# Kernel optimization log

Hardware: AMD Instinct MI355X
Metric: run time of the kernel (lower is better)

Reference implementation:

```python
import jax, jax.numpy as jnp
import numpy as np

B=4; TEXT_LEN=64; IMG=256; P=16; DIM=1024; HEADS=16; LAYERS=2; MLP=4; VOCAB=50000; TDIM=256; MAXTXT=2048
HP=IMG//P; NPATCH=HP*HP; HD=DIM//HEADS; EPS=1e-5

def _ln(x, g, b):
    m = jnp.mean(x, -1, keepdims=True)
    v = jnp.mean((x - m) ** 2, -1, keepdims=True)
    return (x - m) / jnp.sqrt(v + EPS) * g + b

def _rope_cos_sin(n, d):
    inv = 1.0 / (10000.0 ** (jnp.arange(0, d, 2, dtype=jnp.float32) / d))
    f = jnp.outer(jnp.arange(n, dtype=jnp.float32), inv)
    e = jnp.concatenate([f, f], -1)  # [n, d]
    return jnp.cos(e), jnp.sin(e)

def _rot_half(x):
    # matches torch: cat((-x[...,1::2], x[...,::2]), -1)
    return jnp.concatenate([-x[..., 1::2], x[..., ::2]], -1)

def _forward(noisy_images, text_tokens, timesteps, W_tok, pos_text, W_patch, pos_img, cls_tok,
             W_t1, b_t1, W_t2, b_t2, ln1_g, ln1_b, Wq, Wk, Wv, Wo, ln2_g, ln2_b,
             Wm1, Wm2, Wada, b_ada, fn_g, fn_b, W_final, b_final):
    Bn = noisy_images.shape[0]
    # text embed: one_hot @ W_tok.T == gather of columns of W_tok [DIM, VOCAB]
    text_emb = jnp.transpose(jnp.take(W_tok, text_tokens, axis=1), (1, 2, 0)) + pos_text[:, :TEXT_LEN]
    # image patches: [B,3,HP,P,HP,P] -> [B,HP,WP,C,P,P] -> [B,NPATCH, 3*P*P]
    patches = noisy_images.reshape(Bn, 3, HP, P, HP, P).transpose(0, 2, 4, 1, 3, 5).reshape(Bn, NPATCH, 3 * P * P)
    img_emb = patches @ W_patch.T + pos_img
    img_emb = jnp.concatenate([jnp.broadcast_to(cls_tok, (Bn, 1, DIM)), img_emb], 1)
    x = jnp.concatenate([text_emb, img_emb], 1)  # [B, N, DIM]
    N = x.shape[1]
    # sinusoidal timestep embedding (dim=256)
    half = TDIM // 2
    freqs = jnp.exp(-jnp.log(10000.0) * jnp.arange(half, dtype=jnp.float32) / half)
    args = timesteps.astype(jnp.float32)[:, None] * freqs[None]
    temb_raw = jnp.concatenate([jnp.cos(args), jnp.sin(args)], -1)
    t_emb = jax.nn.silu(temb_raw @ W_t1.T + b_t1) @ W_t2.T + b_t2  # [B, DIM]
    cos, sin = _rope_cos_sin(N, HD)
    scale = HD ** -0.5
    for l in range(LAYERS):
        mod = jax.nn.silu(t_emb) @ Wada[l].T + b_ada[l]
        sh_msa, sc_msa, g_msa, sh_mlp, sc_mlp, g_mlp = jnp.split(mod, 6, -1)
        xn = _ln(x, ln1_g[l], ln1_b[l]) * (1 + sc_msa[:, None]) + sh_msa[:, None]
        q = (xn @ Wq[l].T).reshape(Bn, N, HEADS, HD).transpose(0, 2, 1, 3)
        k = (xn @ Wk[l].T).reshape(Bn, N, HEADS, HD).transpose(0, 2, 1, 3)
        v = (xn @ Wv[l].T).reshape(Bn, N, HEADS, HD).transpose(0, 2, 1, 3)
        q = q * cos + _rot_half(q) * sin
        k = k * cos + _rot_half(k) * sin
        att = jax.nn.softmax(jnp.einsum('bhnd,bhmd->bhnm', q, k) * scale, -1)
        o = jnp.einsum('bhnm,bhmd->bhnd', att, v).transpose(0, 2, 1, 3).reshape(Bn, N, DIM)
        x = x + g_msa[:, None] * (o @ Wo[l].T)
        xn2 = _ln(x, ln2_g[l], ln2_b[l]) * (1 + sc_mlp[:, None]) + sh_mlp[:, None]
        mlp = jax.nn.gelu(xn2 @ Wm1[l].T, approximate=False) @ Wm2[l].T
        x = x + g_mlp[:, None] * mlp
    img_tok = x[:, TEXT_LEN + 1:]
    out = _ln(img_tok, fn_g, fn_b) @ W_final.T + b_final  # [B, NPATCH, 3*P*P]
    out = out.reshape(Bn, HP, HP, 3, P, P).transpose(0, 3, 1, 4, 2, 5).reshape(Bn, 3, IMG, IMG)
    return out

def setup_inputs() -> dict:
    key = jax.random.key(0)
    ks = jax.random.split(key, 24)
    def n(k, shape, s=0.02):
        return (jax.random.normal(k, shape, jnp.float32) * s).astype(jnp.float32)
    inp = {}
    inp['noisy_images'] = jax.random.normal(ks[0], (B, 3, IMG, IMG), jnp.float32)
    inp['text_tokens'] = jax.random.randint(ks[1], (B, TEXT_LEN), 0, VOCAB)
    inp['timesteps'] = jax.random.randint(ks[2], (B,), 0, 1000)
    inp['W_tok'] = n(ks[3], (DIM, VOCAB))
    inp['pos_text'] = n(ks[4], (1, MAXTXT, DIM))
    inp['W_patch'] = n(ks[5], (DIM, 3 * P * P))
    inp['pos_img'] = n(ks[6], (1, NPATCH, DIM))
    inp['cls_tok'] = n(ks[7], (1, 1, DIM))
    inp['W_t1'] = n(ks[8], (DIM, TDIM)); inp['b_t1'] = jnp.zeros((DIM,), jnp.float32)
    inp['W_t2'] = n(ks[9], (DIM, DIM)); inp['b_t2'] = jnp.zeros((DIM,), jnp.float32)
    inp['ln1_g'] = jnp.ones((LAYERS, DIM), jnp.float32); inp['ln1_b'] = jnp.zeros((LAYERS, DIM), jnp.float32)
    inp['Wq'] = n(ks[10], (LAYERS, DIM, DIM))
    inp['Wk'] = n(ks[11], (LAYERS, DIM, DIM))
    inp['Wv'] = n(ks[12], (LAYERS, DIM, DIM))
    inp['Wo'] = n(ks[13], (LAYERS, DIM, DIM))
    inp['ln2_g'] = jnp.ones((LAYERS, DIM), jnp.float32); inp['ln2_b'] = jnp.zeros((LAYERS, DIM), jnp.float32)
    inp['Wm1'] = n(ks[14], (LAYERS, MLP * DIM, DIM))
    inp['Wm2'] = n(ks[15], (LAYERS, DIM, MLP * DIM))
    inp['Wada'] = n(ks[16], (LAYERS, 6 * DIM, DIM)); inp['b_ada'] = jnp.zeros((LAYERS, 6 * DIM), jnp.float32)
    inp['fn_g'] = jnp.ones((DIM,), jnp.float32); inp['fn_b'] = jnp.zeros((DIM,), jnp.float32)
    inp['W_final'] = n(ks[17], (3 * P * P, DIM)); inp['b_final'] = jnp.zeros((3 * P * P,), jnp.float32)
    return inp

def reference(noisy_images, text_tokens, timesteps, W_tok, pos_text, W_patch, pos_img, cls_tok,
              W_t1, b_t1, W_t2, b_t2, ln1_g, ln1_b, Wq, Wk, Wv, Wo, ln2_g, ln2_b,
              Wm1, Wm2, Wada, b_ada, fn_g, fn_b, W_final, b_final):
    return _forward(noisy_images, text_tokens, timesteps, W_tok, pos_text, W_patch, pos_img, cls_tok,
                    W_t1, b_t1, W_t2, b_t2, ln1_g, ln1_b, Wq, Wk, Wv, Wo, ln2_g, ln2_b,
                    Wm1, Wm2, Wada, b_ada, fn_g, fn_b, W_final, b_final)
```

## Files before the change

kernel.cpp:

```cpp
#include <hip/hip_runtime.h>
#include <math.h>

constexpr int kBn    = 4;
constexpr int kText  = 64;
constexpr int kImg   = 256;
constexpr int kDim   = 1024;
constexpr int kHeads = 16;
constexpr int kHd    = 64;
constexpr int kNp    = 256;
constexpr int kTok   = 321;
constexpr int kVocab = 50000;
constexpr int kTdim  = 256;
constexpr int kMlp   = 4096;
constexpr int kScLd  = 384;
constexpr int kScRow = 384;
constexpr float kEps = 1e-5f;

typedef __attribute__((ext_vector_type(8))) short short8;
typedef __attribute__((ext_vector_type(4))) float f32x4;

__device__ __forceinline__ short f2bf(float x) {
  unsigned u = __builtin_bit_cast(unsigned, x);
  unsigned r = (u + 0x7FFFu + ((u >> 16) & 1u)) >> 16;
  return (short)r;
}

__device__ __forceinline__ void glds16(const short* g, short* l) {
  __builtin_amdgcn_global_load_lds(
      (const __attribute__((address_space(1))) unsigned int*)g,
      (__attribute__((address_space(3))) unsigned int*)l, 16, 0, 0);
}

struct GemmM {
  const short* A; const short* B; float* C; const float* E;
  int M, N, K, lda, ldb, ldc;
  long sA0, sA1, sB0, sB1, sC0, sC1;
  int innerB, ldE, rowsPB;
  float alpha;
  int nSplit, splitLen;
  long partStride;
};

__device__ __forceinline__ float epi_apply(int EPI, const GemmM& p, const float* E,
                                           long co, int gm, int gn, float v) {
  if (EPI == 1) v += E[gn];
  else if (EPI == 3) v = 0.5f*v*(1.f + erff(v*0.70710678118654752f));
  else if (EPI == 4) v += E[(long)gm*p.ldE + gn];
  else if (EPI == 5) v = p.C[co] + E[(long)(gm / p.rowsPB)*p.ldE + gn] * v;
  return v;
}

template<int EPI, bool PART, bool OUTBF>
__global__ __launch_bounds__(256) void gemm_gl(GemmM p) {
  int bz = blockIdx.z;
  int split = 0;
  if (PART) { split = bz % p.nSplit; bz /= p.nSplit; }
  int b1 = bz % p.innerB, b0 = bz / p.innerB;
  const short* A = p.A + b0*p.sA0 + b1*p.sA1;
  const short* B = p.B + b0*p.sB0 + b1*p.sB1;
  long cbase = b0*p.sC0 + b1*p.sC1 + (PART ? (long)split * p.partStride : 0);
  const float* E = p.E;

  int kBeg = PART ? split * p.splitLen : 0;
  int kEnd = PART ? min(p.K, kBeg + p.splitLen) : p.K;

  __shared__ short As[2][64*64];
  __shared__ short Bs[2][64*64];

  int tid  = threadIdx.x;
  int lane = tid & 63, widx = tid >> 6;
  int quad = lane >> 4, ln = lane & 15;
  int wm = (widx >> 1) * 32, wn = (widx & 1) * 32;
  int n0 = blockIdx.x * 64, m0 = blockIdx.y * 64;

  int l3 = lane >> 3, l7 = lane & 7;
  int kofs = (l7 ^ l3) * 8;
  const short* gA0 = A + (long)(m0 + 16*widx + l3) * p.lda + kofs;
  const short* gA1 = gA0 + (long)8 * p.lda;
  const short* gB0 = B + (long)(n0 + 16*widx + l3) * p.ldb + kofs;
  const short* gB1 = gB0 + (long)8 * p.ldb;
  short* lA0 = &As[0][(2*widx)*512];
  short* lA1 = &As[0][(2*widx+1)*512];
  short* lB0 = &Bs[0][(2*widx)*512];
  short* lB1 = &Bs[0][(2*widx+1)*512];

  auto stage = [&](int buf, int k0) {
    int bo = buf * 4096;
    glds16(gA0 + k0, lA0 + bo);
    glds16(gA1 + k0, lA1 + bo);
    glds16(gB0 + k0, lB0 + bo);
    glds16(gB1 + k0, lB1 + bo);
  };

  f32x4 zero = {0.f, 0.f, 0.f, 0.f};
  f32x4 acc[2][2];
  acc[0][0] = zero; acc[0][1] = zero; acc[1][0] = zero; acc[1][1] = zero;

  stage(0, kBeg);
  int buf = 0;
  for (int k0 = kBeg; k0 < kEnd; k0 += 64) {
    if (k0 + 64 < kEnd) stage(buf ^ 1, k0 + 64);
    __syncthreads();
    const char* Ab = (const char*)&As[buf][0];
    const char* Bb = (const char*)&Bs[buf][0];
#pragma unroll
    for (int ks = 0; ks < 2; ++ks) {
      int cb = ks*64 + quad*16;
      int r0 = wm + ln, r1 = wm + 16 + ln, r2 = wn + ln, r3 = wn + 16 + ln;
      short8 a0 = *(const short8*)(Ab + r0*128 + (cb ^ ((r0 & 7) << 4)));
      short8 a1 = *(const short8*)(Ab + r1*128 + (cb ^ ((r1 & 7) << 4)));
      short8 b0 = *(const short8*)(Bb + r2*128 + (cb ^ ((r2 & 7) << 4)));
      short8 b1 = *(const short8*)(Bb + r3*128 + (cb ^ ((r3 & 7) << 4)));
      acc[0][0] = __builtin_amdgcn_mfma_f32_16x16x32_bf16(a0, b0, acc[0][0], 0, 0, 0);
      acc[0][1] = __builtin_amdgcn_mfma_f32_16x16x32_bf16(a0, b1, acc[0][1], 0, 0, 0);
      acc[1][0] = __builtin_amdgcn_mfma_f32_16x16x32_bf16(a1, b0, acc[1][0], 0, 0, 0);
      acc[1][1] = __builtin_amdgcn_mfma_f32_16x16x32_bf16(a1, b1, acc[1][1], 0, 0, 0);
    }
    __syncthreads();
    buf ^= 1;
  }

#pragma unroll
  for (int mi = 0; mi < 2; ++mi)
#pragma unroll
    for (int ni = 0; ni < 2; ++ni)
#pragma unroll
      for (int reg = 0; reg < 4; ++reg) {
        int gm = m0 + wm + mi*16 + quad*4 + reg;
        int gn = n0 + wn + ni*16 + ln;
        if (gm >= p.M || gn >= p.N) continue;
        long co = cbase + (long)gm * p.ldc + gn;
        float v = acc[mi][ni][reg] * p.alpha;
        if (!PART) v = epi_apply(EPI, p, E, co, gm, gn, v);
        if (OUTBF) ((short*)p.C)[co] = f2bf(v);
        else       p.C[co] = v;
      }
}

template<int EPI, bool PART, bool OUTBF>
__global__ __launch_bounds__(256) void gemm_gl_n128(GemmM p) {
  int bz = blockIdx.z;
  int split = 0;
  if (PART) { split = bz % p.nSplit; bz /= p.nSplit; }
  int b1 = bz % p.innerB, b0 = bz / p.innerB;
  const short* A = p.A + b0*p.sA0 + b1*p.sA1;
  const short* B = p.B + b0*p.sB0 + b1*p.sB1;
  long cbase = b0*p.sC0 + b1*p.sC1 + (PART ? (long)split * p.partStride : 0);
  const float* E = p.E;

  int kBeg = PART ? split * p.splitLen : 0;
  int kEnd = PART ? min(p.K, kBeg + p.splitLen) : p.K;

  __shared__ short As[2][64*64];
  __shared__ short Bs[2][128*64];

  int tid  = threadIdx.x;
  int lane = tid & 63, widx = tid >> 6;
  int quad = lane >> 4, ln = lane & 15;
  int n0 = blockIdx.x * 128, m0 = blockIdx.y * 64;

  int l3 = lane >> 3, l7 = lane & 7;
  int kofs = (l7 ^ l3) * 8;
  const short* gA0 = A + (long)(m0 + 16*widx + l3) * p.lda + kofs;
  const short* gA1 = gA0 + (long)8 * p.lda;
  const short* gB0 = B + (long)(n0 + 32*widx + l3) * p.ldb + kofs;
  const long ldb8 = (long)8 * p.ldb;
  short* lA = &As[0][(2*widx)*512];
  short* lB = &Bs[0][(4*widx)*512];

  auto stage = [&](int buf, int k0) {
    int boA = buf * 4096, boB = buf * 8192;
    glds16(gA0 + k0, lA + boA);
    glds16(gA1 + k0, lA + 512 + boA);
    glds16(gB0 + k0,            lB + boB);
    glds16(gB0 + ldb8 + k0,     lB + 512 + boB);
    glds16(gB0 + 2*ldb8 + k0,   lB + 1024 + boB);
    glds16(gB0 + 3*ldb8 + k0,   lB + 1536 + boB);
  };

  f32x4 zero = {0.f, 0.f, 0.f, 0.f};
  f32x4 acc[4][2];
#pragma unroll
  for (int i = 0; i < 4; ++i) { acc[i][0] = zero; acc[i][1] = zero; }

  stage(0, kBeg);
  int buf = 0;
  for (int k0 = kBeg; k0 < kEnd; k0 += 64) {
    if (k0 + 64 < kEnd) stage(buf ^ 1, k0 + 64);
    __syncthreads();
    const char* Ab = (const char*)&As[buf][0];
    const char* Bb = (const char*)&Bs[buf][0];
#pragma unroll
    for (int ks = 0; ks < 2; ++ks) {
      int cb = ks*64 + quad*16;
      short8 a[4], b[2];
#pragma unroll
      for (int mi = 0; mi < 4; ++mi) {
        int r = mi*16 + ln;
        a[mi] = *(const short8*)(Ab + r*128 + (cb ^ ((r & 7) << 4)));
      }
#pragma unroll
      for (int ni = 0; ni < 2; ++ni) {
        int r = 32*widx + ni*16 + ln;
        b[ni] = *(const short8*)(Bb + r*128 + (cb ^ ((r & 7) << 4)));
      }
#pragma unroll
      for (int mi = 0; mi < 4; ++mi)
#pragma unroll
        for (int ni = 0; ni < 2; ++ni)
          acc[mi][ni] = __builtin_amdgcn_mfma_f32_16x16x32_bf16(a[mi], b[ni], acc[mi][ni], 0, 0, 0);
    }
    __syncthreads();
    buf ^= 1;
  }

#pragma unroll
  for (int mi = 0; mi < 4; ++mi)
#pragma unroll
    for (int ni = 0; ni < 2; ++ni)
#pragma unroll
      for (int reg = 0; reg < 4; ++reg) {
        int gm = m0 + mi*16 + quad*4 + reg;
        int gn = n0 + 32*widx + ni*16 + ln;
        if (gm >= p.M || gn >= p.N) continue;
        long co = cbase + (long)gm * p.ldc + gn;
        float v = acc[mi][ni][reg] * p.alpha;
        if (!PART) v = epi_apply(EPI, p, E, co, gm, gn, v);
        if (OUTBF) ((short*)p.C)[co] = f2bf(v);
        else       p.C[co] = v;
      }
}

static GemmM mkm(const short* A, const short* B, float* C,
                 int M, int N, int K, int lda, int ldb, int ldc) {
  GemmM p; p.A = A; p.B = B; p.C = C; p.E = nullptr;
  p.M = M; p.N = N; p.K = K; p.lda = lda; p.ldb = ldb; p.ldc = ldc;
  p.sA0 = p.sA1 = p.sB0 = p.sB1 = p.sC0 = p.sC1 = 0;
  p.innerB = 1; p.ldE = 0; p.rowsPB = 1; p.alpha = 1.f;
  p.nSplit = 1; p.splitLen = 0; p.partStride = 0;
  return p;
}

static void run_gl(hipStream_t s, int epi, bool outbf, const GemmM& p, int nb) {
  dim3 g((p.N + 63)/64, (p.M + 63)/64, nb), b(256, 1, 1);
  if (outbf) {
    if (epi == 3) gemm_gl<3,false,true><<<g,b,0,s>>>(p);
    else          gemm_gl<0,false,true><<<g,b,0,s>>>(p);
    return;
  }
  switch (epi) {
    case 0: gemm_gl<0,false,false><<<g,b,0,s>>>(p); break;
    case 1: gemm_gl<1,false,false><<<g,b,0,s>>>(p); break;
    case 4: gemm_gl<4,false,false><<<g,b,0,s>>>(p); break;
    case 5: gemm_gl<5,false,false><<<g,b,0,s>>>(p); break;
  }
}

static void run_gl128(hipStream_t s, int epi, bool outbf, const GemmM& p, int nb) {
  dim3 g((p.N + 127)/128, (p.M + 63)/64, nb), b(256, 1, 1);
  if (outbf) {
    if (epi == 3) gemm_gl_n128<3,false,true><<<g,b,0,s>>>(p);
    else          gemm_gl_n128<0,false,true><<<g,b,0,s>>>(p);
    return;
  }
  switch (epi) {
    case 0: gemm_gl_n128<0,false,false><<<g,b,0,s>>>(p); break;
    case 1: gemm_gl_n128<1,false,false><<<g,b,0,s>>>(p); break;
    case 4: gemm_gl_n128<4,false,false><<<g,b,0,s>>>(p); break;
    case 5: gemm_gl_n128<5,false,false><<<g,b,0,s>>>(p); break;
  }
}

static void run_gl128_part(hipStream_t s, const GemmM& p, int nb) {
  dim3 g((p.N + 127)/128, (p.M + 63)/64, nb * p.nSplit), b(256, 1, 1);
  gemm_gl_n128<0,true,false><<<g,b,0,s>>>(p);
}

__global__ __launch_bounds__(256) void reduce_epi4(
    const float* __restrict__ part, long partStride, int S,
    float* __restrict__ C, const float* __restrict__ E,
    int Mv, int Nv, int ldc, long sC0, int ldE, int total) {
  int idx = blockIdx.x*256 + threadIdx.x;
  if (idx >= total) return;
  int n = idx % Nv;
  int m = (idx / Nv) % Mv;
  int b0 = idx / (Nv * Mv);
  long co = b0*sC0 + (long)m*ldc + n;
  float v = 0.f;
  for (int s = 0; s < S; ++s) v += part[(long)s*partStride + co];
  v += E[(long)m*ldE + n];
  C[co] = v;
}

__global__ __launch_bounds__(256) void cvt2_bf16(const float* __restrict__ src,
                                                 short* __restrict__ dst, int n8,
                                                 long srcStride, long dstStride, int total8) {
  int i = blockIdx.x*256 + threadIdx.x;
  if (i >= total8) return;
  int l = i / n8, j = i % n8;
  const float* s = src + srcStride*l + (long)8*j;
  short* d = dst + dstStride*l + (long)8*j;
  float4 a = *(const float4*)s;
  float4 b = *(const float4*)(s + 4);
  short8 o;
  o[0]=f2bf(a.x); o[1]=f2bf(a.y); o[2]=f2bf(a.z); o[3]=f2bf(a.w);
  o[4]=f2bf(b.x); o[5]=f2bf(b.y); o[6]=f2bf(b.z); o[7]=f2bf(b.w);
  *(short8*)d = o;
}

static void cvtT(hipStream_t s, const float* src, short* dst, long nPerLayer,
                 long srcStride, long dstStride, int L) {
  int n8 = (int)(nPerLayer / 8);
  int total8 = n8 * L;
  cvt2_bf16<<<dim3((total8 + 255)/256), dim3(256), 0, s>>>(src, dst, n8, srcStride, dstStride, total8);
}

template<int EPI>
__global__ __launch_bounds__(256) void gemv4(const float* __restrict__ A,
                                             const float* __restrict__ B,
                                             float* __restrict__ C,
                                             const float* __restrict__ bias,
                                             int N, int K, int ldc) {
  int wave = threadIdx.x >> 6, lane = threadIdx.x & 63;
  int n = blockIdx.x * 4 + wave;
  if (n >= N) return;
  const float* Brow = B + (long)n * K;
  float acc0 = 0.f, acc1 = 0.f, acc2 = 0.f, acc3 = 0.f;
  for (int k = lane * 4; k < K; k += 256) {
    float4 b = *(const float4*)(Brow + k);
    float4 a0 = *(const float4*)(A + 0*K + k);
    float4 a1 = *(const float4*)(A + 1*K + k);
    float4 a2 = *(const float4*)(A + 2*K + k);
    float4 a3 = *(const float4*)(A + 3*K + k);
    acc0 += a0.x*b.x + a0.y*b.y + a0.z*b.z + a0.w*b.w;
    acc1 += a1.x*b.x + a1.y*b.y + a1.z*b.z + a1.w*b.w;
    acc2 += a2.x*b.x + a2.y*b.y + a2.z*b.z + a2.w*b.w;
    acc3 += a3.x*b.x + a3.y*b.y + a3.z*b.z + a3.w*b.w;
  }
#pragma unroll
  for (int off = 32; off; off >>= 1) {
    acc0 += __shfl_xor(acc0, off);
    acc1 += __shfl_xor(acc1, off);
    acc2 += __shfl_xor(acc2, off);
    acc3 += __shfl_xor(acc3, off);
  }
  if (lane == 0) {
    float bs = bias[n];
    float v[4] = {acc0 + bs, acc1 + bs, acc2 + bs, acc3 + bs};
#pragma unroll
    for (int m = 0; m < 4; ++m) {
      float x = v[m];
      if (EPI == 2) x = x / (1.f + expf(-x));
      C[(long)m * ldc + n] = x;
    }
  }
}

__global__ void embed_text_cls(const float* __restrict__ Wtok, const int* __restrict__ toks,
                               const float* __restrict__ pos_text, const float* __restrict__ cls_tok,
                               float* __restrict__ x) {
  int idx = blockIdx.x*256 + threadIdx.x;
  int d = idx % kDim;
  int t = (idx / kDim) % (kText + 1);
  int b = idx / (kDim * (kText + 1));
  float v;
  if (t < kText) {
    int tok = toks[b*kText + t];
    v = Wtok[(long)d*kVocab + tok] + pos_text[(long)t*kDim + d];
  } else {
    v = cls_tok[d];
  }
  x[((long)b*kTok + t)*kDim + d] = v;
}

__global__ void extract_patches(const float* __restrict__ img, short* __restrict__ pat) {
  int idx = blockIdx.x*256 + threadIdx.x;
  int k = idx % 768;
  int p = (idx/768) % kNp;
  int b = idx/(768*kNp);
  int c = k >> 8, py = (k >> 4) & 15, px = k & 15;
  int hp = p >> 4, wp = p & 15;
  pat[idx] = f2bf(img[(((long)(b*3 + c))*kImg + hp*16 + py)*kImg + wp*16 + px]);
}

__global__ void time_freqs(const int* __restrict__ ts, float* __restrict__ temb) {
  int b = blockIdx.x, i = threadIdx.x;
  float f = expf(-9.210340371976184f * (float)i / 128.f);
  float a = (float)ts[b] * f;
  temb[b*kTdim + i] = cosf(a);
  temb[b*kTdim + 128 + i] = sinf(a);
}

__global__ void silu_kernel(const float* __restrict__ in, float* __restrict__ outp, int n) {
  int i = blockIdx.x*256 + threadIdx.x;
  if (i < n) { float x = in[i]; outp[i] = x / (1.f + expf(-x)); }
}

__device__ __forceinline__ float block_sum(float v) {
  __shared__ float sh[4];
  for (int off = 32; off; off >>= 1) v += __shfl_down(v, off);
  if ((threadIdx.x & 63) == 0) sh[threadIdx.x >> 6] = v;
  __syncthreads();
  float s = sh[0] + sh[1] + sh[2] + sh[3];
  __syncthreads();
  return s;
}

__global__ __launch_bounds__(256) void ln_mod_kernel(
    const float* __restrict__ x, const float* __restrict__ g, const float* __restrict__ be,
    const float* __restrict__ mod, int shOff, int scOff, short* __restrict__ outp) {
  int row = blockIdx.x;
  int b = row / kTok;
  const float* xr = x + (long)row*kDim;
  float s = 0.f, s2 = 0.f;
  for (int i = threadIdx.x; i < kDim; i += 256) { float v = xr[i]; s += v; s2 += v*v; }
  s = block_sum(s); s2 = block_sum(s2);
  float m = s / kDim;
  float inv = rsqrtf(s2 / kDim - m*m + kEps);
  const float* mb = mod + (long)b*(6*kDim);
  for (int i = threadIdx.x; i < kDim; i += 256) {
    float xn = (xr[i] - m)*inv*g[i] + be[i];
    outp[(long)row*kDim + i] = f2bf(xn*(1.f + mb[scOff + i]) + mb[shOff + i]);
  }
}

__global__ __launch_bounds__(256) void ln_mod_red_kernel(
    const float* __restrict__ xin, const float* __restrict__ part, long pStride, int S,
    const float* __restrict__ gate, const float* __restrict__ g, const float* __restrict__ be,
    const float* __restrict__ mod, int shOff, int scOff,
    float* __restrict__ xout, short* __restrict__ outp) {
  int row = blockIdx.x;
  int b = row / kTok;
  long base = (long)row*kDim;
  const float* gt = gate + (long)b*(6*kDim);
  float v[4];
  float s = 0.f, s2 = 0.f;
#pragma unroll
  for (int c = 0; c < 4; ++c) {
    int i = threadIdx.x + 256*c;
    float acc = 0.f;
    for (int sp = 0; sp < S; ++sp) acc += part[(long)sp*pStride + base + i];
    float xv = xin[base + i] + gt[i] * acc;
    v[c] = xv; s += xv; s2 += xv*xv;
  }
  s = block_sum(s); s2 = block_sum(s2);
  float m = s / kDim;
  float inv = rsqrtf(s2 / kDim - m*m + kEps);
  const float* mb = mod + (long)b*(6*kDim);
#pragma unroll
  for (int c = 0; c < 4; ++c) {
    int i = threadIdx.x + 256*c;
    xout[base + i] = v[c];
    float xn = (v[c] - m)*inv*g[i] + be[i];
    outp[base + i] = f2bf(xn*(1.f + mb[scOff + i]) + mb[shOff + i]);
  }
}

__global__ __launch_bounds__(256) void final_ln_kernel(
    const float* __restrict__ x, const float* __restrict__ g, const float* __restrict__ be,
    short* __restrict__ yn) {
  int row = blockIdx.x;
  int b = row / kNp, p = row % kNp;
  const float* xr = x + ((long)(b*kTok + kText + 1 + p))*kDim;
  float s = 0.f, s2 = 0.f;
  for (int i = threadIdx.x; i < kDim; i += 256) { float v = xr[i]; s += v; s2 += v*v; }
  s = block_sum(s); s2 = block_sum(s2);
  float m = s / kDim;
  float inv = rsqrtf(s2 / kDim - m*m + kEps);
  for (int i = threadIdx.x; i < kDim; i += 256)
    yn[(long)row*kDim + i] = f2bf((xr[i] - m)*inv*g[i] + be[i]);
}

__global__ __launch_bounds__(256) void final_ln_red_kernel(
    const float* __restrict__ xin, const float* __restrict__ part, long pStride, int S,
    const float* __restrict__ gate, const float* __restrict__ g, const float* __restrict__ be,
    short* __restrict__ yn) {
  int row = blockIdx.x;
  int b = row / kNp, p = row % kNp;
  long xb = ((long)(b*kTok + kText + 1 + p))*kDim;
  const float* gt = gate + (long)b*(6*kDim);
  float v[4];
  float s = 0.f, s2 = 0.f;
#pragma unroll
  for (int c = 0; c < 4; ++c) {
    int i = threadIdx.x + 256*c;
    float acc = 0.f;
    for (int sp = 0; sp < S; ++sp) acc += part[(long)sp*pStride + xb + i];
    float xv = xin[xb + i] + gt[i] * acc;
    v[c] = xv; s += xv; s2 += xv*xv;
  }
  s = block_sum(s); s2 = block_sum(s2);
  float m = s / kDim;
  float inv = rsqrtf(s2 / kDim - m*m + kEps);
#pragma unroll
  for (int c = 0; c < 4; ++c) {
    int i = threadIdx.x + 256*c;
    yn[(long)row*kDim + i] = f2bf((v[c] - m)*inv*g[i] + be[i]);
  }
}

__global__ __launch_bounds__(256) void rope_bf16(const float* __restrict__ qkv,
                                                 short* __restrict__ qb,
                                                 short* __restrict__ kb) {
  int idx = blockIdx.x*256 + threadIdx.x;
  int d = idx & (kDim - 1);
  int r = idx >> 10;
  int n = r % kTok;
  int hd = d & 63;
  int j = hd & 31;
  float inv = expf(-9.210340371976184f * (float)j / 32.f);
  float ang = (float)n * inv;
  float c = cosf(ang), s = sinf(ang);
  const float* row = qkv + (long)r * (3*kDim);
  int base = d - hd;
  float qv = row[d], kv = row[kDim + d];
  float qr, kr;
  if (hd < 32) { qr = -row[base + 2*hd + 1];      kr = -row[kDim + base + 2*hd + 1]; }
  else         { qr =  row[base + 2*(hd - 32)];   kr =  row[kDim + base + 2*(hd - 32)]; }
  qb[idx] = f2bf(qv*c + qr*s);
  kb[idx] = f2bf(kv*c + kr*s);
}

__global__ __launch_bounds__(256) void vtrans_t(const float* __restrict__ qkv,
                                                short* __restrict__ vtb) {
  int tt = blockIdx.x;
  int bh = blockIdx.y;
  int b = bh >> 4, h = bh & 15;
  __shared__ float tile[64][65];
  int t = threadIdx.x;
#pragma unroll
  for (int i = 0; i < 16; ++i) {
    int idx = t + 256*i;
    int tok = idx >> 6, d = idx & 63;
    int gtok = tt*64 + tok;
    float v = 0.f;
    if (gtok < kTok) v = qkv[((long)(b*kTok + gtok))*(3*kDim) + 2*kDim + h*kHd + d];
    tile[tok][d] = v;
  }
  __syncthreads();
#pragma unroll
  for (int i = 0; i < 16; ++i) {
    int idx = t + 256*i;
    int d = idx >> 6, tok = idx & 63;
    vtb[((long)bh*kHd + d)*kScLd + tt*64 + tok] = f2bf(tile[tok][d]);
  }
}

__global__ __launch_bounds__(256) void softmax_rows4(float* __restrict__ sc,
                                                     short* __restrict__ scb, int nRows) {
  int wid = threadIdx.x >> 6, t = threadIdx.x & 63;
  int row = blockIdx.x*4 + wid;
  if (row >= nRows) return;
  float* r = sc + (long)row*kScLd;
  int bh = row / kTok, ri = row % kTok;
  short* d = scb + (long)bh*kScRow*kScLd + (long)ri*kScLd;
  float mx = -1e30f;
  for (int i = t; i < kTok; i += 64) mx = fmaxf(mx, r[i]);
  for (int off = 32; off; off >>= 1) mx = fmaxf(mx, __shfl_xor(mx, off));
  float sum = 0.f;
  for (int i = t; i < kTok; i += 64) { float e = expf(r[i] - mx); r[i] = e; sum += e; }
  for (int off = 32; off; off >>= 1) sum += __shfl_xor(sum, off);
  float invs = 1.f / sum;
  for (int i = t; i < kScLd; i += 64)
    d[i] = (i < kTok) ? f2bf(r[i] * invs) : (short)0;
}

__global__ void unpatchify(const float* __restrict__ op, float* __restrict__ outp) {
  int idx = blockIdx.x*256 + threadIdx.x;
  int w = idx & 255;
  int h = (idx >> 8) & 255;
  int c = (idx >> 16) % 3;
  int b = idx / (3 * kImg * kImg);
  int hp = h >> 4, py = h & 15, wp = w >> 4, px = w & 15;
  outp[idx] = op[((long)(b*kNp + hp*16 + wp))*768 + c*256 + py*16 + px];
}

__global__ void unpatchify_red(const float* __restrict__ part, long pStride, int S,
                               const float* __restrict__ bias, float* __restrict__ outp) {
  int idx = blockIdx.x*256 + threadIdx.x;
  int w = idx & 255;
  int h = (idx >> 8) & 255;
  int c = (idx >> 16) % 3;
  int b = idx / (3 * kImg * kImg);
  int hp = h >> 4, py = h & 15, wp = w >> 4, px = w & 15;
  long co = ((long)(b*kNp + hp*16 + wp))*768 + c*256 + py*16 + px;
  float v = bias[c*256 + py*16 + px];
  for (int s = 0; s < S; ++s) v += part[(long)s*pStride + co];
  outp[idx] = v;
}

extern "C" void kernel_launch(void* const* d_in, const int* in_sizes, int n_in,
                              void* d_out, int out_size, void* d_ws, size_t ws_size,
                              hipStream_t stream) {
  (void)in_sizes; (void)n_in; (void)out_size;
  const float* noisy    = (const float*)d_in[0];
  const int*   toks     = (const int*)d_in[1];
  const int*   tsteps   = (const int*)d_in[2];
  const float* W_tok    = (const float*)d_in[3];
  const float* pos_text = (const float*)d_in[4];
  const float* W_patch  = (const float*)d_in[5];
  const float* pos_img  = (const float*)d_in[6];
  const float* cls_tok  = (const float*)d_in[7];
  const float* W_t1     = (const float*)d_in[8];
  const float* b_t1     = (const float*)d_in[9];
  const float* W_t2     = (const float*)d_in[10];
  const float* b_t2     = (const float*)d_in[11];
  const float* ln1_g    = (const float*)d_in[12];
  const float* ln1_b    = (const float*)d_in[13];
  const float* Wq       = (const float*)d_in[14];
  const float* Wk       = (const float*)d_in[15];
  const float* Wv       = (const float*)d_in[16];
  const float* Wo       = (const float*)d_in[17];
  const float* ln2_g    = (const float*)d_in[18];
  const float* ln2_b    = (const float*)d_in[19];
  const float* Wm1      = (const float*)d_in[20];
  const float* Wm2      = (const float*)d_in[21];
  const float* Wada     = (const float*)d_in[22];
  const float* b_ada    = (const float*)d_in[23];
  const float* fn_g     = (const float*)d_in[24];
  const float* fn_b     = (const float*)d_in[25];
  const float* W_final  = (const float*)d_in[26];
  const float* b_final  = (const float*)d_in[27];
  float* out = (float*)d_out;

  float* ws = (float*)d_ws;
  auto alloc = [&](long nf) { float* r = ws; ws += nf; return r; };

  const long seqSz = (long)kBn * kTok * kDim;
  float* x    = alloc(seqSz);
  float* qkv  = alloc((long)kBn*kTok*3*kDim);
  float* sc   = alloc((long)kBn*kHeads*kTok*kScLd);
  short* xnb  = (short*)alloc(seqSz/2);
  short* qb   = (short*)alloc(seqSz/2);
  short* kb   = (short*)alloc(seqSz/2);
  short* ob   = (short*)alloc(seqSz/2);
  short* vtb  = (short*)alloc((long)kBn*kHeads*kHd*kScLd/2);
  short* scb  = (short*)alloc((long)kBn*kHeads*kScRow*kScLd/2);
  short* patb = (short*)alloc((long)kBn*kNp*768/2);
  short* ynb  = (short*)alloc((long)kBn*kNp*kDim/2);
  float* temb = alloc(kBn*kTdim);
  float* t1   = alloc(kBn*kDim);
  float* temb2= alloc(kBn*kDim);
  float* st   = alloc(kBn*kDim);
  float* mod  = alloc(2L*kBn*6*kDim);
  short* hb   = (short*)sc;
  float* outp = qkv;

  const long oPatch = 0;
  const long nPatch = (long)kDim*768;
  const long perLayer = 3L*kDim*kDim + (long)kDim*kDim + 2L*kMlp*kDim;
  const long oLayer = nPatch;
  const long oFinal = nPatch + 2*perLayer;
  const long nFinal = (long)768*kDim;
  short* wAr = (short*)alloc((nPatch + 2*perLayer + nFinal)/2);

  const long scrStride = seqSz;
  float* scr = alloc(4*scrStride);
  bool split_ok = ((char*)ws - (char*)d_ws) <= (long)ws_size;

  cvtT(stream, W_patch, wAr + oPatch, nPatch, 0, 0, 1);
  cvtT(stream, Wq,  wAr + oLayer + 0,               (long)kDim*kDim, (long)kDim*kDim, perLayer, 2);
  cvtT(stream, Wk,  wAr + oLayer + (long)kDim*kDim, (long)kDim*kDim, (long)kDim*kDim, perLayer, 2);
  cvtT(stream, Wv,  wAr + oLayer + 2L*kDim*kDim,    (long)kDim*kDim, (long)kDim*kDim, perLayer, 2);
  cvtT(stream, Wo,  wAr + oLayer + 3L*kDim*kDim,    (long)kDim*kDim, (long)kDim*kDim, perLayer, 2);
  cvtT(stream, Wm1, wAr + oLayer + 4L*kDim*kDim,    (long)kMlp*kDim, (long)kMlp*kDim, perLayer, 2);
  cvtT(stream, Wm2, wAr + oLayer + 4L*kDim*kDim + (long)kMlp*kDim,
       (long)kMlp*kDim, (long)kMlp*kDim, perLayer, 2);
  cvtT(stream, W_final, wAr + oFinal, nFinal, 0, 0, 1);

  embed_text_cls<<<(kBn*(kText+1)*kDim)/256, 256, 0, stream>>>(W_tok, toks, pos_text, cls_tok, x);
  extract_patches<<<(kBn*kNp*768)/256, 256, 0, stream>>>(noisy, patb);
  {
    GemmM p = mkm(patb, wAr + oPatch, split_ok ? scr : (x + (kText+1)*kDim),
                  kNp, kDim, 768, 768, 768, kDim);
    p.sA0 = (long)kNp*768; p.sC0 = (long)kTok*kDim;
    if (split_ok) {
      p.nSplit = 3; p.splitLen = 256; p.partStride = scrStride;
      run_gl128_part(stream, p, kBn);
      int total = kBn*kNp*kDim;
      reduce_epi4<<<(total+255)/256, 256, 0, stream>>>(scr, scrStride, 3,
          x + (kText+1)*kDim, pos_img, kNp, kDim, kDim, (long)kTok*kDim, kDim, total);
    } else {
      p.E = pos_img; p.ldE = kDim;
      run_gl128(stream, 4, false, p, kBn);
    }
  }
  time_freqs<<<kBn, 128, 0, stream>>>(tsteps, temb);
  gemv4<2><<<kDim/4, 256, 0, stream>>>(temb, W_t1, t1, b_t1, kDim, kTdim, kDim);
  gemv4<1><<<kDim/4, 256, 0, stream>>>(t1, W_t2, temb2, b_t2, kDim, kDim, kDim);
  silu_kernel<<<(kBn*kDim + 255)/256, 256, 0, stream>>>(temb2, st, kBn*kDim);
  for (int l = 0; l < 2; ++l)
    gemv4<1><<<(6*kDim)/4, 256, 0, stream>>>(st, Wada + (long)l*6*kDim*kDim,
                                             mod + (long)l*kBn*6*kDim,
                                             b_ada + (long)l*6*kDim, 6*kDim, kDim, 6*kDim);

  ln_mod_kernel<<<kBn*kTok, 256, 0, stream>>>(x, ln1_g, ln1_b, mod, 0, kDim, xnb);

  for (int l = 0; l < 2; ++l) {
    const short* wqkv_l = wAr + oLayer + (long)l*perLayer;
    const short* wo_l   = wqkv_l + 3L*kDim*kDim;
    const short* wm1_l  = wqkv_l + 4L*kDim*kDim;
    const short* wm2_l  = wm1_l + (long)kMlp*kDim;
    float* mod_l = mod + (long)l*kBn*6*kDim;

    {
      GemmM p = mkm(xnb, wqkv_l, qkv, kBn*kTok, 3*kDim, kDim, kDim, kDim, 3*kDim);
      run_gl128(stream, 0, false, p, 1);
    }
    rope_bf16<<<(int)(seqSz/256), 256, 0, stream>>>(qkv, qb, kb);
    vtrans_t<<<dim3(kScLd/64, kBn*kHeads), 256, 0, stream>>>(qkv, vtb);

    {
      GemmM p = mkm(qb, kb, sc, kTok, kTok, kHd, kDim, kDim, kScLd);
      p.sA0 = (long)kTok*kDim; p.sA1 = kHd;
      p.sB0 = (long)kTok*kDim; p.sB1 = kHd;
      p.sC0 = (long)kHeads*kTok*kScLd; p.sC1 = (long)kTok*kScLd;
      p.innerB = kHeads; p.alpha = 0.125f;
      run_gl(stream, 0, false, p, kBn*kHeads);
    }
    {
      int nRows = kBn*kHeads*kTok;
      softmax_rows4<<<(nRows+3)/4, 256, 0, stream>>>(sc, scb, nRows);
    }
    {
      GemmM p = mkm(scb, vtb, (float*)ob, kTok, kHd, kScLd, kScLd, kScLd, kDim);
      p.sA0 = (long)kHeads*kScRow*kScLd; p.sA1 = (long)kScRow*kScLd;
      p.sB0 = (long)kHeads*kHd*kScLd;    p.sB1 = (long)kHd*kScLd;
      p.sC0 = (long)kTok*kDim;           p.sC1 = kHd;
      p.innerB = kHeads;
      run_gl(stream, 0, true, p, kBn*kHeads);
    }
    {
      GemmM p = mkm(ob, wo_l, split_ok ? scr : x, kBn*kTok, kDim, kDim, kDim, kDim, kDim);
      if (split_ok) {
        p.nSplit = 4; p.splitLen = 256; p.partStride = scrStride;
        run_gl128_part(stream, p, 1);
        ln_mod_red_kernel<<<kBn*kTok, 256, 0, stream>>>(x, scr, scrStride, 4,
            mod_l + 2*kDim, ln2_g + l*kDim, ln2_b + l*kDim, mod_l, 3*kDim, 4*kDim, x, xnb);
      } else {
        p.E = mod_l + 2*kDim; p.ldE = 6*kDim; p.rowsPB = kTok;
        run_gl128(stream, 5, false, p, 1);
        ln_mod_kernel<<<kBn*kTok, 256, 0, stream>>>(x, ln2_g + l*kDim, ln2_b + l*kDim,
                                                    mod_l, 3*kDim, 4*kDim, xnb);
      }
    }
    {
      GemmM p = mkm(xnb, wm1_l, (float*)hb, kBn*kTok, kMlp, kDim, kDim, kDim, kMlp);
      run_gl128(stream, 3, true, p, 1);
    }
    {
      GemmM p = mkm(hb, wm2_l, split_ok ? scr : x, kBn*kTok, kDim, kMlp, kMlp, kMlp, kDim);
      if (split_ok) {
        p.nSplit = 4; p.splitLen = 1024; p.partStride = scrStride;
        run_gl128_part(stream, p, 1);
        if (l == 0) {
          ln_mod_red_kernel<<<kBn*kTok, 256, 0, stream>>>(x, scr, scrStride, 4,
              mod_l + 5*kDim, ln1_g + kDim, ln1_b + kDim,
              mod + (long)kBn*6*kDim, 0, kDim, x, xnb);
        } else {
          final_ln_red_kernel<<<kBn*kNp, 256, 0, stream>>>(x, scr, scrStride, 4,
              mod_l + 5*kDim, fn_g, fn_b, ynb);
        }
      } else {
        p.E = mod_l + 5*kDim; p.ldE = 6*kDim; p.rowsPB = kTok;
        run_gl128(stream, 5, false, p, 1);
        if (l == 0)
          ln_mod_kernel<<<kBn*kTok, 256, 0, stream>>>(x, ln1_g + kDim, ln1_b + kDim,
                                                      mod + (long)kBn*6*kDim, 0, kDim, xnb);
        else
          final_ln_kernel<<<kBn*kNp, 256, 0, stream>>>(x, fn_g, fn_b, ynb);
      }
    }
  }

  {
    GemmM p = mkm(ynb, wAr + oFinal, split_ok ? scr : outp, kBn*kNp, 768, kDim, kDim, kDim, 768);
    if (split_ok) {
      p.nSplit = 4; p.splitLen = 256; p.partStride = (long)kBn*kNp*768;
      run_gl128_part(stream, p, 1);
      unpatchify_red<<<(kBn*3*kImg*kImg)/256, 256, 0, stream>>>(scr, (long)kBn*kNp*768, 4,
                                                                b_final, out);
    } else {
      p.E = b_final;
      run_gl128(stream, 1, false, p, 1);
      unpatchify<<<(kBn*3*kImg*kImg)/256, 256, 0, stream>>>(outp, out);
    }
  }
}
```

Before: 786.6 us.

## Fuse attention into flash kernel, batch conversions, merge launches and drop split-K

Replaces the scores GEMM, softmax and PV GEMM with one online-softmax attention kernel per 64-query tile, so the fp32 score matrix is no longer written to and read back from memory. It also merges the weight conversions into a single multi-job kernel, merges embedding with patch extraction and rope with V transpose, and computes both layers' adaLN modulation in one gemv. The final projection now writes straight into the image layout, and the split-K paths for the patch, Wo and final GEMMs are removed. These changes cut launch count and intermediate traffic, but dropping split-K lowers parallelism for those GEMMs, and the attention grid is small (384 blocks).

```diff
diff --git a/kernel.cpp b/kernel.cpp
--- a/kernel.cpp
+++ b/kernel.cpp
@@ -12,11 +12,12 @@
 constexpr int kVocab = 50000;
 constexpr int kTdim  = 256;
 constexpr int kMlp   = 4096;
-constexpr int kScLd  = 384;
-constexpr int kScRow = 384;
+constexpr int kVLd   = 384;
+constexpr int kMod   = 12288;
 constexpr float kEps = 1e-5f;
 
 typedef __attribute__((ext_vector_type(8))) short short8;
+typedef __attribute__((ext_vector_type(4))) short short4v;
 typedef __attribute__((ext_vector_type(4))) float f32x4;
 
 __device__ __forceinline__ short f2bf(float x) {
@@ -40,102 +41,6 @@
   int nSplit, splitLen;
   long partStride;
 };
-
-__device__ __forceinline__ float epi_apply(int EPI, const GemmM& p, const float* E,
-                                           long co, int gm, int gn, float v) {
-  if (EPI == 1) v += E[gn];
-  else if (EPI == 3) v = 0.5f*v*(1.f + erff(v*0.70710678118654752f));
-  else if (EPI == 4) v += E[(long)gm*p.ldE + gn];
-  else if (EPI == 5) v = p.C[co] + E[(long)(gm / p.rowsPB)*p.ldE + gn] * v;
-  return v;
-}
-
-template<int EPI, bool PART, bool OUTBF>
-__global__ __launch_bounds__(256) void gemm_gl(GemmM p) {
-  int bz = blockIdx.z;
-  int split = 0;
-  if (PART) { split = bz % p.nSplit; bz /= p.nSplit; }
-  int b1 = bz % p.innerB, b0 = bz / p.innerB;
-  const short* A = p.A + b0*p.sA0 + b1*p.sA1;
-  const short* B = p.B + b0*p.sB0 + b1*p.sB1;
-  long cbase = b0*p.sC0 + b1*p.sC1 + (PART ? (long)split * p.partStride : 0);
-  const float* E = p.E;
-
-  int kBeg = PART ? split * p.splitLen : 0;
-  int kEnd = PART ? min(p.K, kBeg + p.splitLen) : p.K;
-
-  __shared__ short As[2][64*64];
-  __shared__ short Bs[2][64*64];
-
-  int tid  = threadIdx.x;
-  int lane = tid & 63, widx = tid >> 6;
-  int quad = lane >> 4, ln = lane & 15;
-  int wm = (widx >> 1) * 32, wn = (widx & 1) * 32;
-  int n0 = blockIdx.x * 64, m0 = blockIdx.y * 64;
-
-  int l3 = lane >> 3, l7 = lane & 7;
-  int kofs = (l7 ^ l3) * 8;
-  const short* gA0 = A + (long)(m0 + 16*widx + l3) * p.lda + kofs;
-  const short* gA1 = gA0 + (long)8 * p.lda;
-  const short* gB0 = B + (long)(n0 + 16*widx + l3) * p.ldb + kofs;
-  const short* gB1 = gB0 + (long)8 * p.ldb;
-  short* lA0 = &As[0][(2*widx)*512];
-  short* lA1 = &As[0][(2*widx+1)*512];
-  short* lB0 = &Bs[0][(2*widx)*512];
-  short* lB1 = &Bs[0][(2*widx+1)*512];
-
-  auto stage = [&](int buf, int k0) {
-    int bo = buf * 4096;
-    glds16(gA0 + k0, lA0 + bo);
-    glds16(gA1 + k0, lA1 + bo);
-    glds16(gB0 + k0, lB0 + bo);
-    glds16(gB1 + k0, lB1 + bo);
-  };
-
-  f32x4 zero = {0.f, 0.f, 0.f, 0.f};
-  f32x4 acc[2][2];
-  acc[0][0] = zero; acc[0][1] = zero; acc[1][0] = zero; acc[1][1] = zero;
-
-  stage(0, kBeg);
-  int buf = 0;
-  for (int k0 = kBeg; k0 < kEnd; k0 += 64) {
-    if (k0 + 64 < kEnd) stage(buf ^ 1, k0 + 64);
-    __syncthreads();
-    const char* Ab = (const char*)&As[buf][0];
-    const char* Bb = (const char*)&Bs[buf][0];
-#pragma unroll
-    for (int ks = 0; ks < 2; ++ks) {
-      int cb = ks*64 + quad*16;
-      int r0 = wm + ln, r1 = wm + 16 + ln, r2 = wn + ln, r3 = wn + 16 + ln;
-      short8 a0 = *(const short8*)(Ab + r0*128 + (cb ^ ((r0 & 7) << 4)));
-      short8 a1 = *(const short8*)(Ab + r1*128 + (cb ^ ((r1 & 7) << 4)));
-      short8 b0 = *(const short8*)(Bb + r2*128 + (cb ^ ((r2 & 7) << 4)));
-      short8 b1 = *(const short8*)(Bb + r3*128 + (cb ^ ((r3 & 7) << 4)));
-      acc[0][0] = __builtin_amdgcn_mfma_f32_16x16x32_bf16(a0, b0, acc[0][0], 0, 0, 0);
-      acc[0][1] = __builtin_amdgcn_mfma_f32_16x16x32_bf16(a0, b1, acc[0][1], 0, 0, 0);
-      acc[1][0] = __builtin_amdgcn_mfma_f32_16x16x32_bf16(a1, b0, acc[1][0], 0, 0, 0);
-      acc[1][1] = __builtin_amdgcn_mfma_f32_16x16x32_bf16(a1, b1, acc[1][1], 0, 0, 0);
-    }
-    __syncthreads();
-    buf ^= 1;
-  }
-
-#pragma unroll
-  for (int mi = 0; mi < 2; ++mi)
-#pragma unroll
-    for (int ni = 0; ni < 2; ++ni)
-#pragma unroll
-      for (int reg = 0; reg < 4; ++reg) {
-        int gm = m0 + wm + mi*16 + quad*4 + reg;
-        int gn = n0 + wn + ni*16 + ln;
-        if (gm >= p.M || gn >= p.N) continue;
-        long co = cbase + (long)gm * p.ldc + gn;
-        float v = acc[mi][ni][reg] * p.alpha;
-        if (!PART) v = epi_apply(EPI, p, E, co, gm, gn, v);
-        if (OUTBF) ((short*)p.C)[co] = f2bf(v);
-        else       p.C[co] = v;
-      }
-}
 
 template<int EPI, bool PART, bool OUTBF>
 __global__ __launch_bounds__(256) void gemm_gl_n128(GemmM p) {
@@ -223,9 +128,21 @@
         int gm = m0 + mi*16 + quad*4 + reg;
         int gn = n0 + 32*widx + ni*16 + ln;
         if (gm >= p.M || gn >= p.N) continue;
+        float v = acc[mi][ni][reg] * p.alpha;
+        if (EPI == 6) {
+          int bb = gm >> 8, pp = gm & 255;
+          int cc = gn >> 8, py = (gn >> 4) & 15, px = gn & 15;
+          long oidx = (((long)(bb*3 + cc)*256) + (pp>>4)*16 + py)*256 + (pp&15)*16 + px;
+          p.C[oidx] = v + E[gn];
+          continue;
+        }
         long co = cbase + (long)gm * p.ldc + gn;
-        float v = acc[mi][ni][reg] * p.alpha;
-        if (!PART) v = epi_apply(EPI, p, E, co, gm, gn, v);
+        if (!PART) {
+          if (EPI == 1) v += E[gn];
+          else if (EPI == 3) v = 0.5f*v*(1.f + erff(v*0.70710678118654752f));
+          else if (EPI == 4) v += E[(long)gm*p.ldE + gn];
+          else if (EPI == 5) v = p.C[co] + E[(long)(gm / p.rowsPB)*p.ldE + gn] * v;
+        }
         if (OUTBF) ((short*)p.C)[co] = f2bf(v);
         else       p.C[co] = v;
       }
@@ -241,21 +158,6 @@
   return p;
 }
 
-static void run_gl(hipStream_t s, int epi, bool outbf, const GemmM& p, int nb) {
-  dim3 g((p.N + 63)/64, (p.M + 63)/64, nb), b(256, 1, 1);
-  if (outbf) {
-    if (epi == 3) gemm_gl<3,false,true><<<g,b,0,s>>>(p);
-    else          gemm_gl<0,false,true><<<g,b,0,s>>>(p);
-    return;
-  }
-  switch (epi) {
-    case 0: gemm_gl<0,false,false><<<g,b,0,s>>>(p); break;
-    case 1: gemm_gl<1,false,false><<<g,b,0,s>>>(p); break;
-    case 4: gemm_gl<4,false,false><<<g,b,0,s>>>(p); break;
-    case 5: gemm_gl<5,false,false><<<g,b,0,s>>>(p); break;
-  }
-}
-
 static void run_gl128(hipStream_t s, int epi, bool outbf, const GemmM& p, int nb) {
   dim3 g((p.N + 127)/128, (p.M + 63)/64, nb), b(256, 1, 1);
   if (outbf) {
@@ -268,6 +170,7 @@
     case 1: gemm_gl_n128<1,false,false><<<g,b,0,s>>>(p); break;
     case 4: gemm_gl_n128<4,false,false><<<g,b,0,s>>>(p); break;
     case 5: gemm_gl_n128<5,false,false><<<g,b,0,s>>>(p); break;
+    case 6: gemm_gl_n128<6,false,false><<<g,b,0,s>>>(p); break;
   }
 }
 
@@ -276,43 +179,135 @@
   gemm_gl_n128<0,true,false><<<g,b,0,s>>>(p);
 }
 
-__global__ __launch_bounds__(256) void reduce_epi4(
-    const float* __restrict__ part, long partStride, int S,
-    float* __restrict__ C, const float* __restrict__ E,
-    int Mv, int Nv, int ldc, long sC0, int ldE, int total) {
-  int idx = blockIdx.x*256 + threadIdx.x;
-  if (idx >= total) return;
-  int n = idx % Nv;
-  int m = (idx / Nv) % Mv;
-  int b0 = idx / (Nv * Mv);
-  long co = b0*sC0 + (long)m*ldc + n;
-  float v = 0.f;
-  for (int s = 0; s < S; ++s) v += part[(long)s*partStride + co];
-  v += E[(long)m*ldE + n];
-  C[co] = v;
-}
-
-__global__ __launch_bounds__(256) void cvt2_bf16(const float* __restrict__ src,
-                                                 short* __restrict__ dst, int n8,
-                                                 long srcStride, long dstStride, int total8) {
-  int i = blockIdx.x*256 + threadIdx.x;
-  if (i >= total8) return;
-  int l = i / n8, j = i % n8;
-  const float* s = src + srcStride*l + (long)8*j;
-  short* d = dst + dstStride*l + (long)8*j;
+__global__ __launch_bounds__(256) void attn_fused(
+    const short* __restrict__ qb, const short* __restrict__ kb,
+    const short* __restrict__ vtb, short* __restrict__ ob) {
+  __shared__ short plds[4096];
+  int qt = blockIdx.x, bh = blockIdx.y;
+  int b = bh >> 4, h = bh & 15;
+  int tid = threadIdx.x;
+  int lane = tid & 63, w = tid >> 6;
+  int quad = lane >> 4, ln = lane & 15;
+
+  int gq = qt*64 + w*16 + ln;
+  int gqc = min(gq, kTok - 1);
+  const short* qp = qb + ((long)(b*kTok + gqc))*kDim + h*kHd;
+  short8 qf0 = *(const short8*)(qp + quad*8);
+  short8 qf1 = *(const short8*)(qp + 32 + quad*8);
+
+  const short* kbase = kb + (long)b*kTok*kDim + h*kHd;
+  const short* vbase = vtb + (long)bh*kHd*kVLd;
+  short* pl = &plds[w*1024];
+  int key = (ln & 7) << 2;
+
+  f32x4 zero = {0.f, 0.f, 0.f, 0.f};
+  f32x4 oacc[4];
+#pragma unroll
+  for (int i = 0; i < 4; ++i) oacc[i] = zero;
+  float m_run = -3.0e38f, l_run = 0.f;
+
+  for (int t = 0; t < 6; ++t) {
+    f32x4 st[4];
+#pragma unroll
+    for (int nt = 0; nt < 4; ++nt) {
+      const short* kp = kbase + ((long)min(t*64 + nt*16 + ln, kTok - 1))*kDim;
+      short8 k0 = *(const short8*)(kp + quad*8);
+      short8 k1 = *(const short8*)(kp + 32 + quad*8);
+      f32x4 a = zero;
+      a = __builtin_amdgcn_mfma_f32_16x16x32_bf16(k0, qf0, a, 0, 0, 0);
+      a = __builtin_amdgcn_mfma_f32_16x16x32_bf16(k1, qf1, a, 0, 0, 0);
+      st[nt] = a;
+    }
+#pragma unroll
+    for (int nt = 0; nt < 4; ++nt)
+#pragma unroll
+      for (int reg = 0; reg < 4; ++reg) {
+        int gk = t*64 + nt*16 + quad*4 + reg;
+        float s = st[nt][reg] * 0.125f;
+        st[nt][reg] = (gk < kTok) ? s : -3.0e38f;
+      }
+    float rm = -3.0e38f;
+#pragma unroll
+    for (int nt = 0; nt < 4; ++nt)
+#pragma unroll
+      for (int reg = 0; reg < 4; ++reg) rm = fmaxf(rm, st[nt][reg]);
+    rm = fmaxf(rm, __shfl_xor(rm, 16));
+    rm = fmaxf(rm, __shfl_xor(rm, 32));
+    float m_new = fmaxf(m_run, rm);
+    float scal = expf(m_run - m_new);
+    float rs = 0.f;
+#pragma unroll
+    for (int nt = 0; nt < 4; ++nt)
+#pragma unroll
+      for (int reg = 0; reg < 4; ++reg) {
+        float pv = expf(st[nt][reg] - m_new);
+        st[nt][reg] = pv; rs += pv;
+      }
+    rs += __shfl_xor(rs, 16);
+    rs += __shfl_xor(rs, 32);
+    l_run = l_run * scal + rs;
+    m_run = m_new;
+#pragma unroll
+    for (int dt = 0; dt < 4; ++dt)
+#pragma unroll
+      for (int reg = 0; reg < 4; ++reg) oacc[dt][reg] *= scal;
+
+#pragma unroll
+    for (int nt = 0; nt < 4; ++nt) {
+      unsigned w0 = (unsigned)(unsigned short)f2bf(st[nt][0])
+                  | ((unsigned)(unsigned short)f2bf(st[nt][1]) << 16);
+      unsigned w1 = (unsigned)(unsigned short)f2bf(st[nt][2])
+                  | ((unsigned)(unsigned short)f2bf(st[nt][3]) << 16);
+      int cs = (nt*8 + quad*2) ^ key;
+      uint2 pk; pk.x = w0; pk.y = w1;
+      *(uint2*)(pl + ln*64 + cs*2) = pk;
+    }
+    short8 pf0 = *(const short8*)(pl + ln*64 + (((0*16 + quad*4) ^ key))*2);
+    short8 pf1 = *(const short8*)(pl + ln*64 + (((1*16 + quad*4) ^ key))*2);
+
+#pragma unroll
+    for (int dt = 0; dt < 4; ++dt) {
+      const short* vp = vbase + ((long)(dt*16 + ln))*kVLd + t*64;
+      short8 v0 = *(const short8*)(vp + quad*8);
+      short8 v1 = *(const short8*)(vp + 32 + quad*8);
+      oacc[dt] = __builtin_amdgcn_mfma_f32_16x16x32_bf16(v0, pf0, oacc[dt], 0, 0, 0);
+      oacc[dt] = __builtin_amdgcn_mfma_f32_16x16x32_bf16(v1, pf1, oacc[dt], 0, 0, 0);
+    }
+  }
+
+  if (gq < kTok) {
+    float invl = 1.f / l_run;
+    short* op = ob + ((long)(b*kTok + gq))*kDim + h*kHd;
+#pragma unroll
+    for (int dt = 0; dt < 4; ++dt) {
+      short4v o4;
+#pragma unroll
+      for (int reg = 0; reg < 4; ++reg) o4[reg] = f2bf(oacc[dt][reg] * invl);
+      *(short4v*)(op + dt*16 + quad*4) = o4;
+    }
+  }
+}
+
+struct CvtJobs {
+  const float* src[14];
+  long dstOff[14];
+  long start[14];
+};
+__global__ __launch_bounds__(256) void cvt_all(CvtJobs j, short* __restrict__ dst, int totalG) {
+  int g = blockIdx.x*256 + threadIdx.x;
+  if (g >= totalG) return;
+  int jo = 0;
+#pragma unroll
+  for (int i = 1; i < 14; ++i) if (g >= j.start[i]) jo = i;
+  long lg = g - j.start[jo];
+  const float* s = j.src[jo] + lg*8;
+  short* d = dst + j.dstOff[jo] + lg*8;
   float4 a = *(const float4*)s;
   float4 b = *(const float4*)(s + 4);
   short8 o;
   o[0]=f2bf(a.x); o[1]=f2bf(a.y); o[2]=f2bf(a.z); o[3]=f2bf(a.w);
   o[4]=f2bf(b.x); o[5]=f2bf(b.y); o[6]=f2bf(b.z); o[7]=f2bf(b.w);
   *(short8*)d = o;
-}
-
-static void cvtT(hipStream_t s, const float* src, short* dst, long nPerLayer,
-                 long srcStride, long dstStride, int L) {
-  int n8 = (int)(nPerLayer / 8);
-  int total8 = n8 * L;
-  cvt2_bf16<<<dim3((total8 + 255)/256), dim3(256), 0, s>>>(src, dst, n8, srcStride, dstStride, total8);
 }
 
 template<int EPI>
@@ -356,31 +351,34 @@
   }
 }
 
-__global__ void embed_text_cls(const float* __restrict__ Wtok, const int* __restrict__ toks,
-                               const float* __restrict__ pos_text, const float* __restrict__ cls_tok,
-                               float* __restrict__ x) {
-  int idx = blockIdx.x*256 + threadIdx.x;
-  int d = idx % kDim;
-  int t = (idx / kDim) % (kText + 1);
-  int b = idx / (kDim * (kText + 1));
-  float v;
-  if (t < kText) {
-    int tok = toks[b*kText + t];
-    v = Wtok[(long)d*kVocab + tok] + pos_text[(long)t*kDim + d];
+constexpr int kEmbBlocks = (kBn*(kText+1)*kDim)/256;
+__global__ void embed_patches(const float* __restrict__ Wtok, const int* __restrict__ toks,
+                              const float* __restrict__ pos_text, const float* __restrict__ cls_tok,
+                              float* __restrict__ x,
+                              const float* __restrict__ img, short* __restrict__ pat) {
+  int blk = blockIdx.x;
+  if (blk < kEmbBlocks) {
+    int idx = blk*256 + threadIdx.x;
+    int d = idx % kDim;
+    int t = (idx / kDim) % (kText + 1);
+    int b = idx / (kDim * (kText + 1));
+    float v;
+    if (t < kText) {
+      int tok = toks[b*kText + t];
+      v = Wtok[(long)d*kVocab + tok] + pos_text[(long)t*kDim + d];
+    } else {
+      v = cls_tok[d];
+    }
+    x[((long)b*kTok + t)*kDim + d] = v;
   } else {
-    v = cls_tok[d];
-  }
-  x[((long)b*kTok + t)*kDim + d] = v;
-}
-
-__global__ void extract_patches(const float* __restrict__ img, short* __restrict__ pat) {
-  int idx = blockIdx.x*256 + threadIdx.x;
-  int k = idx % 768;
-  int p = (idx/768) % kNp;
-  int b = idx/(768*kNp);
-  int c = k >> 8, py = (k >> 4) & 15, px = k & 15;
-  int hp = p >> 4, wp = p & 15;
-  pat[idx] = f2bf(img[(((long)(b*3 + c))*kImg + hp*16 + py)*kImg + wp*16 + px]);
+    int idx = (blk - kEmbBlocks)*256 + threadIdx.x;
+    int k = idx % 768;
+    int p = (idx/768) % kNp;
+    int b = idx/(768*kNp);
+    int c = k >> 8, py = (k >> 4) & 15, px = k & 15;
+    int hp = p >> 4, wp = p & 15;
+    pat[idx] = f2bf(img[(((long)(b*3 + c))*kImg + hp*16 + py)*kImg + wp*16 + px]);
+  }
 }
 
 __global__ void time_freqs(const int* __restrict__ ts, float* __restrict__ temb) {
@@ -389,11 +387,6 @@
   float a = (float)ts[b] * f;
   temb[b*kTdim + i] = cosf(a);
   temb[b*kTdim + 128 + i] = sinf(a);
-}
-
-__global__ void silu_kernel(const float* __restrict__ in, float* __restrict__ outp, int n) {
-  int i = blockIdx.x*256 + threadIdx.x;
-  if (i < n) { float x = in[i]; outp[i] = x / (1.f + expf(-x)); }
 }
 
 __device__ __forceinline__ float block_sum(float v) {
@@ -408,7 +401,8 @@
 
 __global__ __launch_bounds__(256) void ln_mod_kernel(
     const float* __restrict__ x, const float* __restrict__ g, const float* __restrict__ be,
-    const float* __restrict__ mod, int shOff, int scOff, short* __restrict__ outp) {
+    const float* __restrict__ mod, int shOff, int scOff, int mStride,
+    short* __restrict__ outp) {
   int row = blockIdx.x;
   int b = row / kTok;
   const float* xr = x + (long)row*kDim;
@@ -417,7 +411,7 @@
   s = block_sum(s); s2 = block_sum(s2);
   float m = s / kDim;
   float inv = rsqrtf(s2 / kDim - m*m + kEps);
-  const float* mb = mod + (long)b*(6*kDim);
+  const float* mb = mod + (long)b*mStride;
   for (int i = threadIdx.x; i < kDim; i += 256) {
     float xn = (xr[i] - m)*inv*g[i] + be[i];
     outp[(long)row*kDim + i] = f2bf(xn*(1.f + mb[scOff + i]) + mb[shOff + i]);
@@ -427,12 +421,12 @@
 __global__ __launch_bounds__(256) void ln_mod_red_kernel(
     const float* __restrict__ xin, const float* __restrict__ part, long pStride, int S,
     const float* __restrict__ gate, const float* __restrict__ g, const float* __restrict__ be,
-    const float* __restrict__ mod, int shOff, int scOff,
+    const float* __restrict__ mod, int shOff, int scOff, int mStride,
     float* __restrict__ xout, short* __restrict__ outp) {
   int row = blockIdx.x;
   int b = row / kTok;
   long base = (long)row*kDim;
-  const float* gt = gate + (long)b*(6*kDim);
+  const float* gt = gate + (long)b*mStride;
   float v[4];
   float s = 0.f, s2 = 0.f;
 #pragma unroll
@@ -446,7 +440,7 @@
   s = block_sum(s); s2 = block_sum(s2);
   float m = s / kDim;
   float inv = rsqrtf(s2 / kDim - m*m + kEps);
-  const float* mb = mod + (long)b*(6*kDim);
+  const float* mb = mod + (long)b*mStride;
 #pragma unroll
   for (int c = 0; c < 4; ++c) {
     int i = threadIdx.x + 256*c;
@@ -474,11 +468,11 @@
 __global__ __launch_bounds__(256) void final_ln_red_kernel(
     const float* __restrict__ xin, const float* __restrict__ part, long pStride, int S,
     const float* __restrict__ gate, const float* __restrict__ g, const float* __restrict__ be,
-    short* __restrict__ yn) {
+    int mStride, short* __restrict__ yn) {
   int row = blockIdx.x;
   int b = row / kNp, p = row % kNp;
   long xb = ((long)(b*kTok + kText + 1 + p))*kDim;
-  const float* gt = gate + (long)b*(6*kDim);
+  const float* gt = gate + (long)b*mStride;
   float v[4];
   float s = 0.f, s2 = 0.f;
 #pragma unroll
@@ -499,94 +493,54 @@
   }
 }
 
-__global__ __launch_bounds__(256) void rope_bf16(const float* __restrict__ qkv,
-                                                 short* __restrict__ qb,
-                                                 short* __restrict__ kb) {
-  int idx = blockIdx.x*256 + threadIdx.x;
-  int d = idx & (kDim - 1);
-  int r = idx >> 10;
-  int n = r % kTok;
-  int hd = d & 63;
-  int j = hd & 31;
-  float inv = expf(-9.210340371976184f * (float)j / 32.f);
-  float ang = (float)n * inv;
-  float c = cosf(ang), s = sinf(ang);
-  const float* row = qkv + (long)r * (3*kDim);
-  int base = d - hd;
-  float qv = row[d], kv = row[kDim + d];
-  float qr, kr;
-  if (hd < 32) { qr = -row[base + 2*hd + 1];      kr = -row[kDim + base + 2*hd + 1]; }
-  else         { qr =  row[base + 2*(hd - 32)];   kr =  row[kDim + base + 2*(hd - 32)]; }
-  qb[idx] = f2bf(qv*c + qr*s);
-  kb[idx] = f2bf(kv*c + kr*s);
-}
-
-__global__ __launch_bounds__(256) void vtrans_t(const float* __restrict__ qkv,
-                                                short* __restrict__ vtb) {
-  int tt = blockIdx.x;
-  int bh = blockIdx.y;
-  int b = bh >> 4, h = bh & 15;
+constexpr int kRopeBlocks = (kBn*kTok*kDim)/256;
+__global__ __launch_bounds__(256) void rope_vtrans(const float* __restrict__ qkv,
+                                                   short* __restrict__ qb,
+                                                   short* __restrict__ kb,
+                                                   short* __restrict__ vtb) {
   __shared__ float tile[64][65];
-  int t = threadIdx.x;
-#pragma unroll
-  for (int i = 0; i < 16; ++i) {
-    int idx = t + 256*i;
-    int tok = idx >> 6, d = idx & 63;
-    int gtok = tt*64 + tok;
-    float v = 0.f;
-    if (gtok < kTok) v = qkv[((long)(b*kTok + gtok))*(3*kDim) + 2*kDim + h*kHd + d];
-    tile[tok][d] = v;
-  }
-  __syncthreads();
-#pragma unroll
-  for (int i = 0; i < 16; ++i) {
-    int idx = t + 256*i;
-    int d = idx >> 6, tok = idx & 63;
-    vtb[((long)bh*kHd + d)*kScLd + tt*64 + tok] = f2bf(tile[tok][d]);
-  }
-}
-
-__global__ __launch_bounds__(256) void softmax_rows4(float* __restrict__ sc,
-                                                     short* __restrict__ scb, int nRows) {
-  int wid = threadIdx.x >> 6, t = threadIdx.x & 63;
-  int row = blockIdx.x*4 + wid;
-  if (row >= nRows) return;
-  float* r = sc + (long)row*kScLd;
-  int bh = row / kTok, ri = row % kTok;
-  short* d = scb + (long)bh*kScRow*kScLd + (long)ri*kScLd;
-  float mx = -1e30f;
-  for (int i = t; i < kTok; i += 64) mx = fmaxf(mx, r[i]);
-  for (int off = 32; off; off >>= 1) mx = fmaxf(mx, __shfl_xor(mx, off));
-  float sum = 0.f;
-  for (int i = t; i < kTok; i += 64) { float e = expf(r[i] - mx); r[i] = e; sum += e; }
-  for (int off = 32; off; off >>= 1) sum += __shfl_xor(sum, off);
-  float invs = 1.f / sum;
-  for (int i = t; i < kScLd; i += 64)
-    d[i] = (i < kTok) ? f2bf(r[i] * invs) : (short)0;
-}
-
-__global__ void unpatchify(const float* __restrict__ op, float* __restrict__ outp) {
-  int idx = blockIdx.x*256 + threadIdx.x;
-  int w = idx & 255;
-  int h = (idx >> 8) & 255;
-  int c = (idx >> 16) % 3;
-  int b = idx / (3 * kImg * kImg);
-  int hp = h >> 4, py = h & 15, wp = w >> 4, px = w & 15;
-  outp[idx] = op[((long)(b*kNp + hp*16 + wp))*768 + c*256 + py*16 + px];
-}
-
-__global__ void unpatchify_red(const float* __restrict__ part, long pStride, int S,
-                               const float* __restrict__ bias, float* __restrict__ outp) {
-  int idx = blockIdx.x*256 + threadIdx.x;
-  int w = idx & 255;
-  int h = (idx >> 8) & 255;
-  int c = (idx >> 16) % 3;
-  int b = idx / (3 * kImg * kImg);
-  int hp = h >> 4, py = h & 15, wp = w >> 4, px = w & 15;
-  long co = ((long)(b*kNp + hp*16 + wp))*768 + c*256 + py*16 + px;
-  float v = bias[c*256 + py*16 + px];
-  for (int s = 0; s < S; ++s) v += part[(long)s*pStride + co];
-  outp[idx] = v;
+  int blk = blockIdx.x;
+  if (blk < kRopeBlocks) {
+    int idx = blk*256 + threadIdx.x;
+    int d = idx & (kDim - 1);
+    int r = idx >> 10;
+    int n = r % kTok;
+    int hd = d & 63;
+    int j = hd & 31;
+    float inv = expf(-9.210340371976184f * (float)j / 32.f);
+    float ang = (float)n * inv;
+    float c = cosf(ang), s = sinf(ang);
+    const float* row = qkv + (long)r * (3*kDim);
+    int base = d - hd;
+    float qv = row[d], kv = row[kDim + d];
+    float qr, kr;
+    if (hd < 32) { qr = -row[base + 2*hd + 1];      kr = -row[kDim + base + 2*hd + 1]; }
+    else         { qr =  row[base + 2*(hd - 32)];   kr =  row[kDim + base + 2*(hd - 32)]; }
+    qb[idx] = f2bf(qv*c + qr*s);
+    kb[idx] = f2bf(kv*c + kr*s);
+  } else {
+    int r = blk - kRopeBlocks;
+    int tt = r % (kVLd/64);
+    int bh = r / (kVLd/64);
+    int b = bh >> 4, h = bh & 15;
+    int t = threadIdx.x;
+#pragma unroll
+    for (int i = 0; i < 16; ++i) {
+      int idx = t + 256*i;
+      int tok = idx >> 6, d = idx & 63;
+      int gtok = tt*64 + tok;
+      float v = 0.f;
+      if (gtok < kTok) v = qkv[((long)(b*kTok + gtok))*(3*kDim) + 2*kDim + h*kHd + d];
+      tile[tok][d] = v;
+    }
+    __syncthreads();
+#pragma unroll
+    for (int i = 0; i < 16; ++i) {
+      int idx = t + 256*i;
+      int d = idx >> 6, tok = idx & 63;
+      vtb[((long)bh*kHd + d)*kVLd + tt*64 + tok] = f2bf(tile[tok][d]);
+    }
+  }
 }
 
 extern "C" void kernel_launch(void* const* d_in, const int* in_sizes, int n_in,
@@ -629,26 +583,21 @@
   const long seqSz = (long)kBn * kTok * kDim;
   float* x    = alloc(seqSz);
   float* qkv  = alloc((long)kBn*kTok*3*kDim);
-  float* sc   = alloc((long)kBn*kHeads*kTok*kScLd);
   short* xnb  = (short*)alloc(seqSz/2);
   short* qb   = (short*)alloc(seqSz/2);
   short* kb   = (short*)alloc(seqSz/2);
   short* ob   = (short*)alloc(seqSz/2);
-  short* vtb  = (short*)alloc((long)kBn*kHeads*kHd*kScLd/2);
-  short* scb  = (short*)alloc((long)kBn*kHeads*kScRow*kScLd/2);
+  short* vtb  = (short*)alloc((long)kBn*kHeads*kHd*kVLd/2);
+  short* hb   = (short*)alloc((long)kBn*kTok*kMlp/2);
   short* patb = (short*)alloc((long)kBn*kNp*768/2);
   short* ynb  = (short*)alloc((long)kBn*kNp*kDim/2);
   float* temb = alloc(kBn*kTdim);
   float* t1   = alloc(kBn*kDim);
-  float* temb2= alloc(kBn*kDim);
   float* st   = alloc(kBn*kDim);
-  float* mod  = alloc(2L*kBn*6*kDim);
-  short* hb   = (short*)sc;
-  float* outp = qkv;
-
-  const long oPatch = 0;
+  float* modC = alloc((long)kBn*kMod);
+
   const long nPatch = (long)kDim*768;
-  const long perLayer = 3L*kDim*kDim + (long)kDim*kDim + 2L*kMlp*kDim;
+  const long perLayer = 4L*kDim*kDim + 2L*kMlp*kDim;
   const long oLayer = nPatch;
   const long oFinal = nPatch + 2*perLayer;
   const long nFinal = (long)768*kDim;
@@ -658,92 +607,64 @@
   float* scr = alloc(4*scrStride);
   bool split_ok = ((char*)ws - (char*)d_ws) <= (long)ws_size;
 
-  cvtT(stream, W_patch, wAr + oPatch, nPatch, 0, 0, 1);
-  cvtT(stream, Wq,  wAr + oLayer + 0,               (long)kDim*kDim, (long)kDim*kDim, perLayer, 2);
-  cvtT(stream, Wk,  wAr + oLayer + (long)kDim*kDim, (long)kDim*kDim, (long)kDim*kDim, perLayer, 2);
-  cvtT(stream, Wv,  wAr + oLayer + 2L*kDim*kDim,    (long)kDim*kDim, (long)kDim*kDim, perLayer, 2);
-  cvtT(stream, Wo,  wAr + oLayer + 3L*kDim*kDim,    (long)kDim*kDim, (long)kDim*kDim, perLayer, 2);
-  cvtT(stream, Wm1, wAr + oLayer + 4L*kDim*kDim,    (long)kMlp*kDim, (long)kMlp*kDim, perLayer, 2);
-  cvtT(stream, Wm2, wAr + oLayer + 4L*kDim*kDim + (long)kMlp*kDim,
-       (long)kMlp*kDim, (long)kMlp*kDim, perLayer, 2);
-  cvtT(stream, W_final, wAr + oFinal, nFinal, 0, 0, 1);
-
-  embed_text_cls<<<(kBn*(kText+1)*kDim)/256, 256, 0, stream>>>(W_tok, toks, pos_text, cls_tok, x);
-  extract_patches<<<(kBn*kNp*768)/256, 256, 0, stream>>>(noisy, patb);
   {
-    GemmM p = mkm(patb, wAr + oPatch, split_ok ? scr : (x + (kText+1)*kDim),
-                  kNp, kDim, 768, 768, 768, kDim);
+    CvtJobs cj;
+    int ji = 0; long cum = 0;
+    auto addJob = [&](const float* s, long off, long n) {
+      cj.src[ji] = s; cj.dstOff[ji] = off; cj.start[ji] = cum; cum += n/8; ++ji;
+    };
+    addJob(W_patch, 0, nPatch);
+    for (int l = 0; l < 2; ++l) {
+      long base = oLayer + (long)l*perLayer;
+      addJob(Wq  + (long)l*kDim*kDim, base + 0,             (long)kDim*kDim);
+      addJob(Wk  + (long)l*kDim*kDim, base + 1L*kDim*kDim,  (long)kDim*kDim);
+      addJob(Wv  + (long)l*kDim*kDim, base + 2L*kDim*kDim,  (long)kDim*kDim);
+      addJob(Wo  + (long)l*kDim*kDim, base + 3L*kDim*kDim,  (long)kDim*kDim);
+      addJob(Wm1 + (long)l*kMlp*kDim, base + 4L*kDim*kDim,  (long)kMlp*kDim);
+      addJob(Wm2 + (long)l*kMlp*kDim, base + 4L*kDim*kDim + (long)kMlp*kDim, (long)kMlp*kDim);
+    }
+    addJob(W_final, oFinal, nFinal);
+    int totalG = (int)cum;
+    cvt_all<<<(totalG + 255)/256, 256, 0, stream>>>(cj, wAr, totalG);
+  }
+
+  embed_patches<<<kEmbBlocks + (kBn*kNp*768)/256, 256, 0, stream>>>(
+      W_tok, toks, pos_text, cls_tok, x, noisy, patb);
+  {
+    GemmM p = mkm(patb, wAr, x + (kText+1)*kDim, kNp, kDim, 768, 768, 768, kDim);
     p.sA0 = (long)kNp*768; p.sC0 = (long)kTok*kDim;
-    if (split_ok) {
-      p.nSplit = 3; p.splitLen = 256; p.partStride = scrStride;
-      run_gl128_part(stream, p, kBn);
-      int total = kBn*kNp*kDim;
-      reduce_epi4<<<(total+255)/256, 256, 0, stream>>>(scr, scrStride, 3,
-          x + (kText+1)*kDim, pos_img, kNp, kDim, kDim, (long)kTok*kDim, kDim, total);
-    } else {
-      p.E = pos_img; p.ldE = kDim;
-      run_gl128(stream, 4, false, p, kBn);
-    }
+    p.E = pos_img; p.ldE = kDim;
+    run_gl128(stream, 4, false, p, kBn);
   }
   time_freqs<<<kBn, 128, 0, stream>>>(tsteps, temb);
   gemv4<2><<<kDim/4, 256, 0, stream>>>(temb, W_t1, t1, b_t1, kDim, kTdim, kDim);
-  gemv4<1><<<kDim/4, 256, 0, stream>>>(t1, W_t2, temb2, b_t2, kDim, kDim, kDim);
-  silu_kernel<<<(kBn*kDim + 255)/256, 256, 0, stream>>>(temb2, st, kBn*kDim);
-  for (int l = 0; l < 2; ++l)
-    gemv4<1><<<(6*kDim)/4, 256, 0, stream>>>(st, Wada + (long)l*6*kDim*kDim,
-                                             mod + (long)l*kBn*6*kDim,
-                                             b_ada + (long)l*6*kDim, 6*kDim, kDim, 6*kDim);
-
-  ln_mod_kernel<<<kBn*kTok, 256, 0, stream>>>(x, ln1_g, ln1_b, mod, 0, kDim, xnb);
+  gemv4<2><<<kDim/4, 256, 0, stream>>>(t1, W_t2, st, b_t2, kDim, kDim, kDim);
+  gemv4<1><<<kMod/4, 256, 0, stream>>>(st, Wada, modC, b_ada, kMod, kDim, kMod);
+
+  ln_mod_kernel<<<kBn*kTok, 256, 0, stream>>>(x, ln1_g, ln1_b, modC, 0, kDim, kMod, xnb);
 
   for (int l = 0; l < 2; ++l) {
     const short* wqkv_l = wAr + oLayer + (long)l*perLayer;
     const short* wo_l   = wqkv_l + 3L*kDim*kDim;
     const short* wm1_l  = wqkv_l + 4L*kDim*kDim;
     const short* wm2_l  = wm1_l + (long)kMlp*kDim;
-    float* mod_l = mod + (long)l*kBn*6*kDim;
+    const float* mod_l  = modC + (long)l*6*kDim;
 
     {
       GemmM p = mkm(xnb, wqkv_l, qkv, kBn*kTok, 3*kDim, kDim, kDim, kDim, 3*kDim);
       run_gl128(stream, 0, false, p, 1);
     }
-    rope_bf16<<<(int)(seqSz/256), 256, 0, stream>>>(qkv, qb, kb);
-    vtrans_t<<<dim3(kScLd/64, kBn*kHeads), 256, 0, stream>>>(qkv, vtb);
+    rope_vtrans<<<kRopeBlocks + (kVLd/64)*kBn*kHeads, 256, 0, stream>>>(qkv, qb, kb, vtb);
+
+    attn_fused<<<dim3(6, kBn*kHeads), 256, 0, stream>>>(qb, kb, vtb, ob);
 
     {
-      GemmM p = mkm(qb, kb, sc, kTok, kTok, kHd, kDim, kDim, kScLd);
-      p.sA0 = (long)kTok*kDim; p.sA1 = kHd;
-      p.sB0 = (long)kTok*kDim; p.sB1 = kHd;
-      p.sC0 = (long)kHeads*kTok*kScLd; p.sC1 = (long)kTok*kScLd;
-      p.innerB = kHeads; p.alpha = 0.125f;
-      run_gl(stream, 0, false, p, kBn*kHeads);
-    }
-    {
-      int nRows = kBn*kHeads*kTok;
-      softmax_rows4<<<(nRows+3)/4, 256, 0, stream>>>(sc, scb, nRows);
-    }
-    {
-      GemmM p = mkm(scb, vtb, (float*)ob, kTok, kHd, kScLd, kScLd, kScLd, kDim);
-      p.sA0 = (long)kHeads*kScRow*kScLd; p.sA1 = (long)kScRow*kScLd;
-      p.sB0 = (long)kHeads*kHd*kScLd;    p.sB1 = (long)kHd*kScLd;
-      p.sC0 = (long)kTok*kDim;           p.sC1 = kHd;
-      p.innerB = kHeads;
-      run_gl(stream, 0, true, p, kBn*kHeads);
-    }
-    {
-      GemmM p = mkm(ob, wo_l, split_ok ? scr : x, kBn*kTok, kDim, kDim, kDim, kDim, kDim);
-      if (split_ok) {
-        p.nSplit = 4; p.splitLen = 256; p.partStride = scrStride;
-        run_gl128_part(stream, p, 1);
-        ln_mod_red_kernel<<<kBn*kTok, 256, 0, stream>>>(x, scr, scrStride, 4,
-            mod_l + 2*kDim, ln2_g + l*kDim, ln2_b + l*kDim, mod_l, 3*kDim, 4*kDim, x, xnb);
-      } else {
-        p.E = mod_l + 2*kDim; p.ldE = 6*kDim; p.rowsPB = kTok;
-        run_gl128(stream, 5, false, p, 1);
-        ln_mod_kernel<<<kBn*kTok, 256, 0, stream>>>(x, ln2_g + l*kDim, ln2_b + l*kDim,
-                                                    mod_l, 3*kDim, 4*kDim, xnb);
-      }
-    }
+      GemmM p = mkm(ob, wo_l, x, kBn*kTok, kDim, kDim, kDim, kDim, kDim);
+      p.E = mod_l + 2*kDim; p.ldE = kMod; p.rowsPB = kTok;
+      run_gl128(stream, 5, false, p, 1);
+    }
+    ln_mod_kernel<<<kBn*kTok, 256, 0, stream>>>(x, ln2_g + l*kDim, ln2_b + l*kDim,
+                                                mod_l, 3*kDim, 4*kDim, kMod, xnb);
     {
       GemmM p = mkm(xnb, wm1_l, (float*)hb, kBn*kTok, kMlp, kDim, kDim, kDim, kMlp);
       run_gl128(stream, 3, true, p, 1);
@@ -756,17 +677,17 @@
         if (l == 0) {
           ln_mod_red_kernel<<<kBn*kTok, 256, 0, stream>>>(x, scr, scrStride, 4,
               mod_l + 5*kDim, ln1_g + kDim, ln1_b + kDim,
-              mod + (long)kBn*6*kDim, 0, kDim, x, xnb);
+              modC + 6*kDim, 0, kDim, kMod, x, xnb);
         } else {
           final_ln_red_kernel<<<kBn*kNp, 256, 0, stream>>>(x, scr, scrStride, 4,
-              mod_l + 5*kDim, fn_g, fn_b, ynb);
+              mod_l + 5*kDim, fn_g, fn_b, kMod, ynb);
         }
       } else {
-        p.E = mod_l + 5*kDim; p.ldE = 6*kDim; p.rowsPB = kTok;
+        p.E = mod_l + 5*kDim; p.ldE = kMod; p.rowsPB = kTok;
         run_gl128(stream, 5, false, p, 1);
         if (l == 0)
           ln_mod_kernel<<<kBn*kTok, 256, 0, stream>>>(x, ln1_g + kDim, ln1_b + kDim,
-                                                      mod + (long)kBn*6*kDim, 0, kDim, xnb);
+                                                      modC + 6*kDim, 0, kDim, kMod, xnb);
         else
           final_ln_kernel<<<kBn*kNp, 256, 0, stream>>>(x, fn_g, fn_b, ynb);
       }
@@ -774,16 +695,8 @@
   }
 
   {
-    GemmM p = mkm(ynb, wAr + oFinal, split_ok ? scr : outp, kBn*kNp, 768, kDim, kDim, kDim, 768);
-    if (split_ok) {
-      p.nSplit = 4; p.splitLen = 256; p.partStride = (long)kBn*kNp*768;
-      run_gl128_part(stream, p, 1);
-      unpatchify_red<<<(kBn*3*kImg*kImg)/256, 256, 0, stream>>>(scr, (long)kBn*kNp*768, 4,
-                                                                b_final, out);
-    } else {
-      p.E = b_final;
-      run_gl128(stream, 1, false, p, 1);
-      unpatchify<<<(kBn*3*kImg*kImg)/256, 256, 0, stream>>>(outp, out);
-    }
-  }
-}
+    GemmM p = mkm(ynb, wAr + oFinal, out, kBn*kNp, 768, kDim, kDim, kDim, 768);
+    p.E = b_final;
+    run_gl128(stream, 6, false, p, 1);
+  }
+}
```

Result: faster. 758.8 us (-3.5%).
